# Kernel tuning notes

Measured on AMD Instinct MI355X. Metric: run time of the kernel, lower is better.

## Reference

```python
import jax, jax.numpy as jnp
import numpy as np

B_, S_, D_ = 2, 1024, 1024
EXPAND = 2
D_INNER = EXPAND * D_            # 2048
HEADDIM = 64
NHEADS = D_INNER // HEADDIM      # 32
D_STATE = 64
NGROUPS = 1
D_CONV = 4
CONV_DIM = D_INNER + 2 * NGROUPS * D_STATE      # 2176
D_IN_PROJ = 2 * D_INNER + 2 * NGROUPS * D_STATE + NHEADS  # 4256
H_MLP = 8 * D_                   # GatedMLP fc_1 out (scale * d_model)


def setup_inputs() -> dict:
    key = jax.random.key(0)
    ks = jax.random.split(key, 12)
    n = lambda k, shp, s=0.02: jax.random.normal(k, shp, dtype=jnp.float32) * s
    return {
        "x": jax.random.normal(ks[0], (B_, S_, D_), dtype=jnp.float32),
        "in_proj_w": n(ks[1], (D_IN_PROJ, D_)),
        "conv_w": n(ks[2], (CONV_DIM, D_CONV), 0.2),
        "conv_b": jnp.zeros((CONV_DIM,), jnp.float32),
        "dt_bias": jax.random.normal(ks[3], (NHEADS,), dtype=jnp.float32) * 0.5 - 2.0,
        "A_log": jnp.log(1.0 + 15.0 * jax.random.uniform(ks[4], (NHEADS,), dtype=jnp.float32)),
        "D": jax.random.normal(ks[5], (NHEADS,), dtype=jnp.float32) * 0.1 + 1.0,
        "ssm_norm_w": jnp.ones((D_INNER,), jnp.float32),
        "out_proj_w": n(ks[6], (D_, D_INNER)),
        "rms_w": jnp.ones((D_,), jnp.float32),
        "fc1_w": n(ks[7], (H_MLP, D_)),
        "fc2_w": n(ks[8], (D_, H_MLP // 2)),
    }


def _rms(x, w, eps=1e-5):
    return x * jax.lax.rsqrt(jnp.mean(x * x, axis=-1, keepdims=True) + eps) * w


def _mamba(x, in_proj_w, conv_w, conv_b, dt_bias, A_log, D, ssm_norm_w, out_proj_w):
    b, s, _ = x.shape
    zxbcdt = x @ in_proj_w.T                         # [b,s,D_IN_PROJ]
    z = zxbcdt[..., :D_INNER]
    xBC = zxbcdt[..., D_INNER:D_INNER + CONV_DIM]
    dt_raw = zxbcdt[..., -NHEADS:]
    # causal depthwise conv1d + SiLU
    xc = jnp.pad(jnp.transpose(xBC, (0, 2, 1)), ((0, 0), (0, 0), (D_CONV - 1, 0)))
    xc = jax.lax.conv_general_dilated(xc, conv_w[:, None, :], (1,), 'VALID',
                                      feature_group_count=CONV_DIM,
                                      dimension_numbers=('NCH', 'OIH', 'NCH'))
    xBC = jax.nn.silu(jnp.transpose(xc, (0, 2, 1)) + conv_b)
    xs = xBC[..., :D_INNER].reshape(b, s, NHEADS, HEADDIM)
    Bm = xBC[..., D_INNER:D_INNER + D_STATE]         # [b,s,n] (ngroups=1)
    Cm = xBC[..., D_INNER + D_STATE:]
    dt = jax.nn.softplus(dt_raw + dt_bias)           # [b,s,h]
    dA = jnp.exp(dt * (-jnp.exp(A_log)))             # [b,s,h]
    dtx = dt[..., None] * xs                          # [b,s,h,p]

    def step(h, inp):
        dA_t, dtx_t, B_t, C_t = inp
        h = h * dA_t[:, :, None, None] + jnp.einsum('bhp,bn->bhpn', dtx_t, B_t)
        y = jnp.einsum('bhpn,bn->bhp', h, C_t)
        return h, y

    h0 = jnp.zeros((b, NHEADS, HEADDIM, D_STATE), x.dtype)
    _, y = jax.lax.scan(step, h0, (jnp.transpose(dA, (1, 0, 2)),
                                   jnp.transpose(dtx, (1, 0, 2, 3)),
                                   jnp.transpose(Bm, (1, 0, 2)),
                                   jnp.transpose(Cm, (1, 0, 2))))
    y = jnp.transpose(y, (1, 0, 2, 3)) + D[None, None, :, None] * xs
    y = y.reshape(b, s, D_INNER) * jax.nn.silu(z)    # gated
    y = _rms(y, ssm_norm_w)
    return y @ out_proj_w.T


def reference(x, in_proj_w, conv_w, conv_b, dt_bias, A_log, D, ssm_norm_w,
              out_proj_w, rms_w, fc1_w, fc2_w):
    # x = x + mamba(x)
    x = x + _mamba(x, in_proj_w, conv_w, conv_b, dt_bias, A_log, D, ssm_norm_w, out_proj_w)
    # x = x + GatedMLP(RMSNorm(x))
    xn = _rms(x, rms_w)
    h1 = xn @ fc1_w.T
    a, g = jnp.split(h1, 2, axis=-1)
    m = (a * jax.nn.silu(g)) @ fc2_w.T
    return x + m
```

## Files before the change

kernel.cpp:

```cpp
#include <hip/hip_runtime.h>
#include <math.h>

typedef unsigned short u16;
typedef __attribute__((ext_vector_type(8))) __bf16 bf16x8;
typedef __attribute__((ext_vector_type(4))) float f32x4;
typedef __attribute__((ext_vector_type(4))) u16 u16x4;
typedef __attribute__((ext_vector_type(8))) u16 u16x8;
typedef __attribute__((ext_vector_type(4))) float float4v;

constexpr int kS = 1024;
constexpr int kD = 1024;
constexpr int kDinner = 2048;
constexpr int kHeads = 32;
constexpr int kConvDim = 2176;
constexpr int kDproj = 4256;
constexpr int kDprojPad = 4352;
constexpr int kRows = 2048;
constexpr int kHmlp = 8192;
constexpr int kHhalf = 4096;
constexpr int kL = 64;
constexpr int kNC = 16;

__device__ __forceinline__ float bf2f(u16 u) {
    return __builtin_bit_cast(float, (unsigned int)u << 16);
}
__device__ __forceinline__ u16 f2bf(float f) {
    unsigned int u = __builtin_bit_cast(unsigned int, f);
    u += 0x7fffu + ((u >> 16) & 1u);
    return (u16)(u >> 16);
}
__device__ __forceinline__ float silu_(float x) { return x / (1.f + __expf(-x)); }

__device__ __forceinline__ void gld16(const u16* g, u16* l) {
    __builtin_amdgcn_global_load_lds(
        (const __attribute__((address_space(1))) void*)g,
        (__attribute__((address_space(3))) void*)l, 16, 0, 0);
}

constexpr int kB1 = kRows * kD / 4;
constexpr int kB2 = kB1 + kDprojPad * kD / 4;
constexpr int kB3 = kB2 + kD * kDinner / 4;
constexpr int kB4 = kB3 + kHmlp * kD / 4;
constexpr int kB5 = kB4 + kD * kHhalf / 4;
__global__ __launch_bounds__(256)
void cast_all_kernel(const float* __restrict__ x, const float* __restrict__ w1,
                     const float* __restrict__ w2, const float* __restrict__ w3,
                     const float* __restrict__ w4, u16* __restrict__ xbf,
                     u16* __restrict__ w1bf, u16* __restrict__ w2bf,
                     u16* __restrict__ w3bf, u16* __restrict__ w4bf) {
    int i = blockIdx.x * 256 + threadIdx.x;
    const float* src;
    u16* dst;
    int j;
    if (i < kB1) {
        j = i; src = x; dst = xbf;
    } else if (i < kB2) {
        j = i - kB1;
        int e = j * 4, row = e >> 10, col = e & 1023;
        u16x4 o = {0, 0, 0, 0};
        if (row < kDproj) {
            float4v v = *(const float4v*)(w1 + (size_t)row * kD + col);
            o.x = f2bf(v.x); o.y = f2bf(v.y); o.z = f2bf(v.z); o.w = f2bf(v.w);
        }
        ((u16x4*)w1bf)[j] = o;
        return;
    } else if (i < kB3) {
        j = i - kB2; src = w2; dst = w2bf;
    } else if (i < kB4) {
        j = i - kB3;
        int e = j * 4, row = e >> 10, col4 = (e & 1023) >> 2;
        int p = (row < kHhalf) ? row : row - kHhalf;
        int permrow = (p >> 4) * 32 + (p & 15) + ((row < kHhalf) ? 0 : 16);
        float4v v = ((const float4v*)w3)[j];
        u16x4 o;
        o.x = f2bf(v.x); o.y = f2bf(v.y); o.z = f2bf(v.z); o.w = f2bf(v.w);
        ((u16x4*)w3bf)[permrow * 256 + col4] = o;
        return;
    } else {
        j = i - kB4; src = w4; dst = w4bf;
    }
    float4v v = ((const float4v*)src)[j];
    u16x4 o;
    o.x = f2bf(v.x); o.y = f2bf(v.y); o.z = f2bf(v.z); o.w = f2bf(v.w);
    ((u16x4*)dst)[j] = o;
}

template <bool OUT_BF16, bool GATED = false>
__global__ __launch_bounds__(256)
void gemm_bt(const u16* __restrict__ A, const u16* __restrict__ W,
             void* __restrict__ Cout, const float* __restrict__ resid,
             int M, int N, int K) {
    __shared__ u16 As[2][128 * 32];
    __shared__ u16 Bs[2][128 * 32];
    const int tid = threadIdx.x;
    const int lane = tid & 63;
    const int w = __builtin_amdgcn_readfirstlane(tid >> 6);
    const int wm = w >> 1, wn = w & 1;
    const int bm = blockIdx.y * 128;
    const int bn = blockIdx.x * 128;
    const int z = blockIdx.z;
    const int Kchunk = K / gridDim.z;
    const int k0 = z * Kchunk;

    f32x4 acc[4][4];
#pragma unroll
    for (int i = 0; i < 4; i++)
#pragma unroll
        for (int j = 0; j < 4; j++) acc[i][j] = {0.f, 0.f, 0.f, 0.f};

    const int srow = lane >> 2;
    const int scol = (lane & 3) * 8;
    const u16* gA = A + (size_t)(bm + w * 32 + srow) * K + k0 + scol;
    const u16* gB = W + (size_t)(bn + w * 32 + srow) * K + k0 + scol;
    const size_t rstep = (size_t)16 * K;

    const int sbase0 = (w * 32) * 32;
    const int sbase1 = (w * 32 + 16) * 32;
    const int fra = (lane & 15) * 32 + (lane >> 4) * 8;

    gld16(gA, &As[0][sbase0]);
    gld16(gA + rstep, &As[0][sbase1]);
    gld16(gB, &Bs[0][sbase0]);
    gld16(gB + rstep, &Bs[0][sbase1]);

    const int nk = Kchunk >> 5;
    for (int i = 0; i < nk; i++) {
        const int cur = i & 1, nxt = cur ^ 1;
        __syncthreads();
        if (i + 1 < nk) {
            int kt2 = (i + 1) * 32;
            gld16(gA + kt2, &As[nxt][sbase0]);
            gld16(gA + kt2 + rstep, &As[nxt][sbase1]);
            gld16(gB + kt2, &Bs[nxt][sbase0]);
            gld16(gB + kt2 + rstep, &Bs[nxt][sbase1]);
        }
        bf16x8 av[4], bv[4];
#pragma unroll
        for (int mi = 0; mi < 4; mi++)
            av[mi] = *(const bf16x8*)&As[cur][(wm * 64 + mi * 16) * 32 + fra];
#pragma unroll
        for (int ni = 0; ni < 4; ni++)
            bv[ni] = *(const bf16x8*)&Bs[cur][(wn * 64 + ni * 16) * 32 + fra];
#pragma unroll
        for (int mi = 0; mi < 4; mi++)
#pragma unroll
            for (int ni = 0; ni < 4; ni++)
                acc[mi][ni] = __builtin_amdgcn_mfma_f32_16x16x32_bf16(av[mi], bv[ni], acc[mi][ni], 0, 0, 0);
    }

    const int rb = bm + wm * 64 + ((lane >> 4) << 2);
    const int cb = bn + wn * 64 + (lane & 15);
    if (GATED) {
        u16* Cb = (u16*)Cout;
        const int NG = N >> 1;
        const int gc0 = ((bn + wn * 64) >> 1) + (lane & 15);
#pragma unroll
        for (int mi = 0; mi < 4; mi++) {
#pragma unroll
            for (int p = 0; p < 2; p++) {
#pragma unroll
                for (int r = 0; r < 4; r++) {
                    float a = acc[mi][2 * p][r];
                    float g = acc[mi][2 * p + 1][r];
                    Cb[(size_t)(rb + mi * 16 + r) * NG + gc0 + p * 16] =
                        f2bf(a * silu_(g));
                }
            }
        }
        return;
    }
    float* Cf = (float*)Cout + (size_t)z * M * N;
    u16* Cb = (u16*)Cout;
#pragma unroll
    for (int mi = 0; mi < 4; mi++) {
#pragma unroll
        for (int ni = 0; ni < 4; ni++) {
#pragma unroll
            for (int r = 0; r < 4; r++) {
                size_t offo = (size_t)(rb + mi * 16 + r) * N + (cb + ni * 16);
                float v = acc[mi][ni][r];
                if (resid) v += resid[offo];
                if (OUT_BF16) Cb[offo] = f2bf(v);
                else Cf[offo] = v;
            }
        }
    }
}

#define VMCNT6 asm volatile("s_waitcnt vmcnt(6)" ::: "memory")
#define VMCNT0 asm volatile("s_waitcnt vmcnt(0)" ::: "memory")

__global__ __launch_bounds__(512, 2)
void gemm256_gated(const u16* __restrict__ A, const u16* __restrict__ W,
                   u16* __restrict__ Cout, int M, int N, int K) {
    __shared__ u16 lds[2][2][2][2][4096];
    const int tid = threadIdx.x;
    const int lane = tid & 63;
    const int w = __builtin_amdgcn_readfirstlane(tid >> 6);
    const int wm = w >> 2;
    const int wn = w & 3;
    const int wnh = wn >> 1, wnl = wn & 1;

    const int ntn = N >> 8;
    const int ntiles = (M >> 8) * ntn;
    const int qchunk = ntiles >> 3;
    const int lin = blockIdx.x;
    const int swz = (lin & 7) * qchunk + (lin >> 3);
    const int bm = (swz / ntn) << 8;
    const int bn = (swz % ntn) << 8;

    const int rst = tid >> 2, sst = tid & 3;
    const int vst = (((rst >> 1) & 1) << 1) | ((rst >> 2) & 1);
    const u16* gA0 = A + (size_t)(bm + rst) * K + ((sst ^ vst) << 3);
    const u16* gB0 = W + (size_t)(bn + rst) * K + ((sst ^ vst) << 3);
    const size_t hstep = (size_t)128 * K;
    const int wq512 = w * 512;

    const int r0a = lane & 15, slot = lane >> 4;
    const int v2a = (((r0a >> 1) & 1) << 1) | ((r0a >> 2) & 1);
    const int fro = r0a * 32 + ((slot ^ v2a) << 3);

    f32x4 acc[8][4];
#pragma unroll
    for (int i = 0; i < 8; i++)
#pragma unroll
        for (int j = 0; j < 4; j++) acc[i][j] = {0.f, 0.f, 0.f, 0.f};
    bf16x8 bv[4];
    const int nt = K >> 6;

#define STAGE(d, mat, kh, kt)                                               \
    { const u16* g_ = ((mat) ? gB0 : gA0) + (size_t)(kt) * 64 + (kh) * 32;  \
      gld16(g_, &lds[d][mat][0][kh][wq512]);                                \
      gld16(g_ + hstep, &lds[d][mat][1][kh][wq512]); }

#define LDA_FRAG(dst, d, kh, mfb)                                           \
    _Pragma("unroll") for (int i_ = 0; i_ < 4; i_++)                        \
        dst[i_] = *(const bf16x8*)&lds[d][0][wm][kh][((mfb) + i_) * 512 + fro];

#define LDB_FRAG(d, kh)                                                     \
    _Pragma("unroll") for (int i_ = 0; i_ < 4; i_++)                        \
        bv[i_] = *(const bf16x8*)&lds[d][1][wnh][kh][wnl * 2048 + i_ * 512 + fro];

#define PHASE_TAIL(g4)                                                      \
    __builtin_amdgcn_sched_barrier(0);                                      \
    __builtin_amdgcn_s_barrier();                                           \
    __builtin_amdgcn_sched_barrier(0);                                      \
    __builtin_amdgcn_s_setprio(1);                                          \
    _Pragma("unroll") for (int i_ = 0; i_ < 4; i_++)                        \
        _Pragma("unroll") for (int n_ = 0; n_ < 4; n_++)                    \
            acc[(g4) * 4 + i_][n_] = __builtin_amdgcn_mfma_f32_16x16x32_bf16( \
                av[i_], bv[n_], acc[(g4) * 4 + i_][n_], 0, 0, 0);           \
    __builtin_amdgcn_s_setprio(0);                                          \
    __builtin_amdgcn_sched_barrier(0);                                      \
    __builtin_amdgcn_s_barrier();                                           \
    __builtin_amdgcn_sched_barrier(0);

#define TILE(T, D)                                                          \
    {                                             \
      { bf16x8 av[4]; LDB_FRAG(D, 0); LDA_FRAG(av, D, 0, 0);                \
        if ((T) + 1 < nt) STAGE(D ^ 1, 0, 1, (T) + 1);                      \
        PHASE_TAIL(0) }                                                     \
                                                  \
      { bf16x8 av[4]; LDA_FRAG(av, D, 0, 4);                                \
        if ((T) + 2 < nt) STAGE(D, 1, 0, (T) + 2);                          \
        PHASE_TAIL(1) }                                                     \
                                                  \
      { bf16x8 av[4]; LDB_FRAG(D, 1); LDA_FRAG(av, D, 1, 0);                \
        if ((T) + 2 < nt) STAGE(D, 0, 0, (T) + 2);                          \
        PHASE_TAIL(0) }                                                     \
                                  \
      { bf16x8 av[4]; LDA_FRAG(av, D, 1, 4);                                \
        if ((T) + 2 < nt) STAGE(D, 1, 1, (T) + 2);                          \
        if ((T) + 2 < nt) { VMCNT6; } else if ((T) + 1 < nt) { VMCNT0; }    \
        PHASE_TAIL(1) }                                                     \
    }

    STAGE(0, 1, 0, 0);
    STAGE(0, 0, 0, 0);
    STAGE(0, 1, 1, 0);
    STAGE(0, 0, 1, 0);
    STAGE(1, 1, 0, 1);
    STAGE(1, 0, 0, 1);
    STAGE(1, 1, 1, 1);
    VMCNT6;
    __builtin_amdgcn_sched_barrier(0);
    __builtin_amdgcn_s_barrier();
    __builtin_amdgcn_sched_barrier(0);

    for (int tt = 0; tt < nt; tt += 2) {
        TILE(tt, 0)
        TILE(tt + 1, 1)
    }

#undef TILE
#undef PHASE_TAIL
#undef LDB_FRAG
#undef LDA_FRAG
#undef STAGE

    u16* Cb = Cout;
    const int NG = N >> 1;
    const int rb = bm + wm * 128 + ((lane >> 4) << 2);
    const int gc0 = ((bn + wn * 64) >> 1) + (lane & 15);
#pragma unroll
    for (int mf = 0; mf < 8; mf++) {
#pragma unroll
        for (int p = 0; p < 2; p++) {
#pragma unroll
            for (int r = 0; r < 4; r++) {
                float a = acc[mf][2 * p][r];
                float g = acc[mf][2 * p + 1][r];
                Cb[(size_t)(rb + mf * 16 + r) * NG + gc0 + p * 16] =
                    f2bf(a * silu_(g));
            }
        }
    }
}

__global__ __launch_bounds__(256)
void splitk_reduce_kernel(const float* __restrict__ Cp, const float* __restrict__ resid,
                          float* __restrict__ out, int mn4) {
    int i = blockIdx.x * 256 + threadIdx.x;
    if (i >= mn4) return;
    constexpr size_t MN = (size_t)kRows * kD;
    float4v s0 = ((const float4v*)Cp)[i];
    float4v s1 = ((const float4v*)(Cp + MN))[i];
    float4v s2 = ((const float4v*)(Cp + 2 * MN))[i];
    float4v s3 = ((const float4v*)(Cp + 3 * MN))[i];
    float4v r = ((const float4v*)resid)[i];
    float4v o;
    o.x = s0.x + s1.x + s2.x + s3.x + r.x;
    o.y = s0.y + s1.y + s2.y + s3.y + r.y;
    o.z = s0.z + s1.z + s2.z + s3.z + r.z;
    o.w = s0.w + s1.w + s2.w + s3.w + r.w;
    ((float4v*)out)[i] = o;
}

__global__ __launch_bounds__(256)
void reduce_rms_kernel(const float* __restrict__ Cp, const float* __restrict__ resid,
                       float* __restrict__ x2, const float* __restrict__ rmsw,
                       u16* __restrict__ xnbf) {
    const int row = blockIdx.x;
    const int tid = threadIdx.x;
    constexpr size_t MN = (size_t)kRows * kD;
    size_t i = (size_t)row * (kD / 4) + tid;
    float4v s0 = ((const float4v*)Cp)[i];
    float4v s1 = ((const float4v*)(Cp + MN))[i];
    float4v s2 = ((const float4v*)(Cp + 2 * MN))[i];
    float4v s3 = ((const float4v*)(Cp + 3 * MN))[i];
    float4v r = ((const float4v*)resid)[i];
    float4v v;
    v.x = s0.x + s1.x + s2.x + s3.x + r.x;
    v.y = s0.y + s1.y + s2.y + s3.y + r.y;
    v.z = s0.z + s1.z + s2.z + s3.z + r.z;
    v.w = s0.w + s1.w + s2.w + s3.w + r.w;
    ((float4v*)x2)[i] = v;
    float ss = v.x * v.x + v.y * v.y + v.z * v.z + v.w * v.w;
#pragma unroll
    for (int off = 32; off > 0; off >>= 1) ss += __shfl_down(ss, off);
    __shared__ float red[4];
    int wv = tid >> 6, lane = tid & 63;
    if (lane == 0) red[wv] = ss;
    __syncthreads();
    ss = red[0] + red[1] + red[2] + red[3];
    float rstd = rsqrtf(ss * (1.f / kD) + 1e-5f);
    float4v wv4 = ((const float4v*)rmsw)[tid];
    u16x4 o;
    o.x = f2bf(v.x * rstd * wv4.x);
    o.y = f2bf(v.y * rstd * wv4.y);
    o.z = f2bf(v.z * rstd * wv4.z);
    o.w = f2bf(v.w * rstd * wv4.w);
    ((u16x4*)xnbf)[i] = o;
}

__global__ __launch_bounds__(256)
void convdt_kernel(const u16* __restrict__ zxbf, const float* __restrict__ convw,
                   const float* __restrict__ convb, u16* __restrict__ xsbf,
                   float* __restrict__ BCf, const float* __restrict__ dt_bias,
                   const float* __restrict__ A_log, float* __restrict__ dtf,
                   float* __restrict__ dAf) {
    int c = blockIdx.x * 256 + threadIdx.x;
    int row = blockIdx.y;
    if (c >= kConvDim + kHeads) return;
    if (c < kConvDim) {
        int s = row & (kS - 1);
        float acc = convb[c];
#pragma unroll
        for (int j = 0; j < 4; j++) {
            int sj = s - 3 + j;
            if (sj >= 0)
                acc += bf2f(zxbf[(size_t)(row - 3 + j) * kDprojPad + kDinner + c]) * convw[c * 4 + j];
        }
        float v = silu_(acc);
        if (c < kDinner) xsbf[(size_t)row * kDinner + c] = f2bf(v);
        else BCf[(size_t)row * 128 + (c - kDinner)] = v;
    } else {
        int h = c - kConvDim;
        float raw = bf2f(zxbf[(size_t)row * kDprojPad + (kDinner + kConvDim) + h]) + dt_bias[h];
        float dt = (raw > 20.f) ? raw : log1pf(__expf(raw));
        float dA = __expf(-dt * __expf(A_log[h]));
        dtf[(size_t)row * kHeads + h] = dt;
        dAf[(size_t)row * kHeads + h] = dA;
    }
}

__global__ __launch_bounds__(256)
void scan_chunk_kernel(const u16* __restrict__ xsbf, const float* __restrict__ BCf,
                       const float* __restrict__ dtf, const float* __restrict__ dAf,
                       const float* __restrict__ Dv, u16* __restrict__ ysbf,
                       float* __restrict__ Pf, float* __restrict__ Scf) {
    const int c = blockIdx.x, h = blockIdx.y, b = blockIdx.z;
    const int tid = threadIdx.x;
    const int lane = tid & 63;
    const int nq = tid >> 6;
    const int p = nq * 16 + (lane & 15);
    const int ng = lane >> 4;

    __shared__ float BC_lds[kL * 136];
    __shared__ u16 xs_lds[kL * 64];
    __shared__ float dA_lds[kL];
    __shared__ float dt_lds[kL];
    __shared__ u16 ybuf[kL * 64];

    const int row0 = b * kS + c * kL;

#pragma unroll
    for (int i = 0; i < 8; i++) {
        int e4 = i * 256 + tid;
        int t = e4 >> 5;
        int col = (e4 & 31) * 4;
        float4v v = *(const float4v*)(BCf + (size_t)(row0 + t) * 128 + col);
        int dst = t * 136 + (col < 64 ? col : col + 4);
        *(float4v*)&BC_lds[dst] = v;
    }
#pragma unroll
    for (int i = 0; i < 2; i++) {
        int e8 = i * 256 + tid;
        int t = e8 >> 3, col8 = (e8 & 7) * 8;
        *(u16x8*)&xs_lds[t * 64 + col8] =
            *(const u16x8*)(xsbf + (size_t)(row0 + t) * kDinner + h * 64 + col8);
    }
    if (tid < kL) {
        dt_lds[tid] = dtf[(size_t)(row0 + tid) * kHeads + h];
        dA_lds[tid] = dAf[(size_t)(row0 + tid) * kHeads + h];
    }
    __syncthreads();

    float hst[16];
#pragma unroll
    for (int j = 0; j < 16; j++) hst[j] = 0.f;
    float P = 1.f;
    const float Dh = Dv[h];

    for (int t = 0; t < kL; t++) {
        float dAv = dA_lds[t];
        float dtv = dt_lds[t];
        float xsv = bf2f(xs_lds[t * 64 + p]);
        float dtx = dtv * xsv;
        P *= dAv;
        const float* Bt = &BC_lds[t * 136 + ng * 16];
        const float* Ct = Bt + 68;
        float yp = 0.f;
#pragma unroll
        for (int j = 0; j < 16; j++) {
            float Bn = Bt[j];
            float Cn = Ct[j];
            hst[j] = hst[j] * dAv + dtx * Bn;
            yp += hst[j] * Cn;
        }
        yp += __shfl_xor(yp, 16);
        yp += __shfl_xor(yp, 32);
        if (ng == 0) ybuf[t * 64 + p] = f2bf(yp + Dh * xsv);
        if (tid == 0) Pf[(size_t)(row0 + t) * kHeads + h] = P;
    }
    __syncthreads();

#pragma unroll
    for (int i = 0; i < 2; i++) {
        int e8 = i * 256 + tid;
        int t = e8 >> 3, col8 = (e8 & 7) * 8;
        *(u16x8*)(ysbf + (size_t)(row0 + t) * kDinner + h * 64 + col8) =
            *(u16x8*)&ybuf[t * 64 + col8];
    }
    const int bhc = (b * 32 + h) * kNC + c;
    float* Sdst = Scf + (size_t)bhc * 4096 + p * 64 + ng * 16;
#pragma unroll
    for (int j = 0; j < 16; j += 4) {
        f32x4 v = {hst[j], hst[j + 1], hst[j + 2], hst[j + 3]};
        *(f32x4*)(Sdst + j) = v;
    }
}

__global__ __launch_bounds__(256)
void chunk_state_kernel(const float* __restrict__ Scf, const float* __restrict__ Pf,
                        float* __restrict__ Hinf) {
    const int bh = blockIdx.x;
    const int b = bh >> 5, h = bh & 31;
    const int tid = threadIdx.x;
    float hreg[16];
#pragma unroll
    for (int k = 0; k < 16; k++) hreg[k] = 0.f;
    for (int c = 0; c < kNC - 1; c++) {
        float Q = Pf[(size_t)(b * kS + c * kL + kL - 1) * kHeads + h];
        size_t sbase = (size_t)(bh * kNC + c) * 4096;
        size_t dbase = (size_t)(bh * kNC + c + 1) * 4096;
#pragma unroll
        for (int k = 0; k < 16; k++) {
            float s = Scf[sbase + k * 256 + tid];
            hreg[k] = Q * hreg[k] + s;
            Hinf[dbase + k * 256 + tid] = hreg[k];
        }
    }
}

__global__ __launch_bounds__(256)
void chunk_corr_kernel(const float* __restrict__ Hinf, const float* __restrict__ BCf,
                       const float* __restrict__ Pf, u16* __restrict__ ysbf) {
    const int c = blockIdx.x + 1;
    const int h = blockIdx.y, b = blockIdx.z;
    const int tid = threadIdx.x;
    const int lane = tid & 63, wq = tid >> 6;
    __shared__ float Hin_lds[64 * 65];
    __shared__ float C_lds[kL * 64];
    const int bh = b * 32 + h;
    const size_t hbase = (size_t)(bh * kNC + c) * 4096;
#pragma unroll
    for (int k = 0; k < 16; k++) {
        int e = k * 256 + tid;
        Hin_lds[(e >> 6) * 65 + (e & 63)] = Hinf[hbase + e];
    }
    const int row0 = b * kS + c * kL;
#pragma unroll
    for (int k = 0; k < 4; k++) {
        int e4 = k * 256 + tid;
        int t = e4 >> 4, n4 = (e4 & 15) * 4;
        *(float4v*)&C_lds[t * 64 + n4] =
            *(const float4v*)(BCf + (size_t)(row0 + t) * 128 + 64 + n4);
    }
    __syncthreads();

    float hr[64];
#pragma unroll
    for (int n = 0; n < 64; n++) hr[n] = Hin_lds[lane * 65 + n];

    for (int tt = 0; tt < 16; tt++) {
        int t = wq * 16 + tt;
        float corr = 0.f;
#pragma unroll
        for (int n4 = 0; n4 < 16; n4++) {
            float4v cv = *(const float4v*)&C_lds[t * 64 + n4 * 4];
            corr += cv.x * hr[n4 * 4] + cv.y * hr[n4 * 4 + 1] +
                    cv.z * hr[n4 * 4 + 2] + cv.w * hr[n4 * 4 + 3];
        }
        float Pt = Pf[(size_t)(row0 + t) * kHeads + h];
        size_t yoff = (size_t)(row0 + t) * kDinner + h * 64 + lane;
        ysbf[yoff] = f2bf(bf2f(ysbf[yoff]) + Pt * corr);
    }
}

__global__ __launch_bounds__(256)
void gatenorm_kernel(const u16* __restrict__ ysbf, const u16* __restrict__ zxbf,
                     const float* __restrict__ normw, u16* __restrict__ ybf) {
    const int row = blockIdx.x;
    const int tid = threadIdx.x;
    float v[8];
    float ss = 0.f;
#pragma unroll
    for (int i = 0; i < 8; i++) {
        int idx = i * 256 + tid;
        float y = bf2f(ysbf[(size_t)row * kDinner + idx]);
        float z = bf2f(zxbf[(size_t)row * kDprojPad + idx]);
        v[i] = y * silu_(z);
        ss += v[i] * v[i];
    }
#pragma unroll
    for (int off = 32; off > 0; off >>= 1) ss += __shfl_down(ss, off);
    __shared__ float red[4];
    int wv = tid >> 6, lane = tid & 63;
    if (lane == 0) red[wv] = ss;
    __syncthreads();
    ss = red[0] + red[1] + red[2] + red[3];
    float rstd = rsqrtf(ss * (1.f / kDinner) + 1e-5f);
#pragma unroll
    for (int i = 0; i < 8; i++) {
        int idx = i * 256 + tid;
        ybf[(size_t)row * kDinner + idx] = f2bf(v[i] * rstd * normw[idx]);
    }
}

extern "C" void kernel_launch(void* const* d_in, const int* in_sizes, int n_in,
                              void* d_out, int out_size, void* d_ws, size_t ws_size,
                              hipStream_t stream) {
    const float* x         = (const float*)d_in[0];
    const float* in_proj_w = (const float*)d_in[1];
    const float* conv_w    = (const float*)d_in[2];
    const float* conv_b    = (const float*)d_in[3];
    const float* dt_bias   = (const float*)d_in[4];
    const float* A_log     = (const float*)d_in[5];
    const float* Dvec      = (const float*)d_in[6];
    const float* ssm_norm_w= (const float*)d_in[7];
    const float* out_proj_w= (const float*)d_in[8];
    const float* rms_w     = (const float*)d_in[9];
    const float* fc1_w     = (const float*)d_in[10];
    const float* fc2_w     = (const float*)d_in[11];
    float* out = (float*)d_out;

    char* ws = (char*)d_ws;
    size_t off = 0;
    auto alloc = [&](size_t bytes) -> void* {
        void* p = ws + off;
        off += (bytes + 255) & ~(size_t)255;
        return p;
    };
    u16*   xbf  = (u16*)alloc((size_t)kRows * kD * 2);
    u16*   w1bf = (u16*)alloc((size_t)kDprojPad * kD * 2);
    u16*   w2bf = (u16*)alloc((size_t)kD * kDinner * 2);
    u16*   w3bf = (u16*)alloc((size_t)kHmlp * kD * 2);
    u16*   w4bf = (u16*)alloc((size_t)kD * kHhalf * 2);
    u16*   zxbf = (u16*)alloc((size_t)kRows * kDprojPad * 2);
    u16*   xsbf = (u16*)alloc((size_t)kRows * kDinner * 2);
    float* BCf  = (float*)alloc((size_t)kRows * 128 * 4);
    float* dtf  = (float*)alloc((size_t)kRows * kHeads * 4);
    float* dAf  = (float*)alloc((size_t)kRows * kHeads * 4);
    float* Pf   = (float*)alloc((size_t)kRows * kHeads * 4);
    u16*   ysbf = (u16*)alloc((size_t)kRows * kDinner * 2);
    u16*   ybf  = (u16*)alloc((size_t)kRows * kDinner * 2);
    float* x2   = (float*)alloc((size_t)kRows * kD * 4);
    u16*   xnbf = (u16*)alloc((size_t)kRows * kD * 2);
    u16*   h1bf = (u16*)alloc((size_t)kRows * kHmlp * 2);
    u16*   gbf  = (u16*)alloc((size_t)kRows * kHhalf * 2);
    float* Scf  = (float*)gbf;
    float* Hinf = (float*)h1bf;
    float* Cp   = (float*)h1bf;
    (void)ws_size; (void)in_sizes; (void)n_in; (void)out_size;

    cast_all_kernel<<<kB5 / 256, 256, 0, stream>>>(
        x, in_proj_w, out_proj_w, fc1_w, fc2_w, xbf, w1bf, w2bf, w3bf, w4bf);

    gemm_bt<true><<<dim3(kDprojPad / 128, kRows / 128, 1), 256, 0, stream>>>(
        xbf, w1bf, zxbf, nullptr, kRows, kDprojPad, kD);

    convdt_kernel<<<dim3((kConvDim + kHeads + 255) / 256, kRows), 256, 0, stream>>>(
        zxbf, conv_w, conv_b, xsbf, BCf, dt_bias, A_log, dtf, dAf);

    scan_chunk_kernel<<<dim3(kNC, kHeads, 2), 256, 0, stream>>>(
        xsbf, BCf, dtf, dAf, Dvec, ysbf, Pf, Scf);
    chunk_state_kernel<<<64, 256, 0, stream>>>(Scf, Pf, Hinf);
    chunk_corr_kernel<<<dim3(kNC - 1, kHeads, 2), 256, 0, stream>>>(Hinf, BCf, Pf, ysbf);

    gatenorm_kernel<<<kRows, 256, 0, stream>>>(ysbf, zxbf, ssm_norm_w, ybf);

    gemm_bt<false><<<dim3(kD / 128, kRows / 128, 4), 256, 0, stream>>>(
        ybf, w2bf, Cp, nullptr, kRows, kD, kDinner);
    reduce_rms_kernel<<<kRows, 256, 0, stream>>>(Cp, x, x2, rms_w, xnbf);

    gemm256_gated<<<dim3((kRows >> 8) * (kHmlp >> 8)), 512, 0, stream>>>(
        xnbf, w3bf, gbf, kRows, kHmlp, kD);

    gemm_bt<false><<<dim3(kD / 128, kRows / 128, 4), 256, 0, stream>>>(
        gbf, w4bf, Cp, nullptr, kRows, kD, kHhalf);
    splitk_reduce_kernel<<<(kRows * kD / 4 + 255) / 256, 256, 0, stream>>>(
        Cp, x2, out, kRows * kD / 4);
}
```

Baseline: 372.0 us.

## Relax gated GEMM pipeline waits, drop sched barriers, remap tiles per XCD

The gated fc1 GEMM's software pipeline is reworked. Global-load waits move after the MFMA block and are loosened (vmcnt 10 instead of 6), with an extra wait in the second phase. Explicit lgkmcnt waits replace the sched_barrier fences, so the compiler can interleave more freely. The block-to-tile mapping is also changed to a fixed 2D XCD-aware layout so each XCD works on a compact 4x8 tile region for L2 reuse. The intent is more overlap of loads with MFMAs and better cache locality. The risks are a hardcoded grid shape and possible data races if the vmcnt accounting is wrong.

```diff
diff --git a/kernel.cpp b/kernel.cpp
--- a/kernel.cpp
+++ b/kernel.cpp
@@ -187,8 +187,8 @@
     }
 }
 
-#define VMCNT6 asm volatile("s_waitcnt vmcnt(6)" ::: "memory")
-#define VMCNT0 asm volatile("s_waitcnt vmcnt(0)" ::: "memory")
+#define VMCNT10 asm volatile("s_waitcnt vmcnt(10)" ::: "memory")
+#define VMCNT0  asm volatile("s_waitcnt vmcnt(0)" ::: "memory")
 
 __global__ __launch_bounds__(512, 2)
 void gemm256_gated(const u16* __restrict__ A, const u16* __restrict__ W,
@@ -201,13 +201,10 @@
     const int wn = w & 3;
     const int wnh = wn >> 1, wnl = wn & 1;
 
-    const int ntn = N >> 8;
-    const int ntiles = (M >> 8) * ntn;
-    const int qchunk = ntiles >> 3;
     const int lin = blockIdx.x;
-    const int swz = (lin & 7) * qchunk + (lin >> 3);
-    const int bm = (swz / ntn) << 8;
-    const int bn = (swz % ntn) << 8;
+    const int xcd = lin & 7, j = lin >> 3;
+    const int bm = (((xcd >> 2) << 2) + (j & 3)) << 8;
+    const int bn = (((xcd & 3) << 3) + (j >> 2)) << 8;
 
     const int rst = tid >> 2, sst = tid & 3;
     const int vst = (((rst >> 1) & 1) << 1) | ((rst >> 2) & 1);
@@ -224,7 +221,7 @@
 #pragma unroll
     for (int i = 0; i < 8; i++)
 #pragma unroll
-        for (int j = 0; j < 4; j++) acc[i][j] = {0.f, 0.f, 0.f, 0.f};
+        for (int j_ = 0; j_ < 4; j_++) acc[i][j_] = {0.f, 0.f, 0.f, 0.f};
     bf16x8 bv[4];
     const int nt = K >> 6;
 
@@ -241,38 +238,36 @@
     _Pragma("unroll") for (int i_ = 0; i_ < 4; i_++)                        \
         bv[i_] = *(const bf16x8*)&lds[d][1][wnh][kh][wnl * 2048 + i_ * 512 + fro];
 
-#define PHASE_TAIL(g4)                                                      \
-    __builtin_amdgcn_sched_barrier(0);                                      \
+#define PHASE_TAIL(g4, ...)                                                 \
     __builtin_amdgcn_s_barrier();                                           \
-    __builtin_amdgcn_sched_barrier(0);                                      \
+    asm volatile("s_waitcnt lgkmcnt(0)" ::: "memory");                      \
     __builtin_amdgcn_s_setprio(1);                                          \
     _Pragma("unroll") for (int i_ = 0; i_ < 4; i_++)                        \
         _Pragma("unroll") for (int n_ = 0; n_ < 4; n_++)                    \
             acc[(g4) * 4 + i_][n_] = __builtin_amdgcn_mfma_f32_16x16x32_bf16( \
                 av[i_], bv[n_], acc[(g4) * 4 + i_][n_], 0, 0, 0);           \
     __builtin_amdgcn_s_setprio(0);                                          \
-    __builtin_amdgcn_sched_barrier(0);                                      \
-    __builtin_amdgcn_s_barrier();                                           \
-    __builtin_amdgcn_sched_barrier(0);
+    __VA_ARGS__;                                                            \
+    __builtin_amdgcn_s_barrier();
 
 #define TILE(T, D)                                                          \
     {                                             \
       { bf16x8 av[4]; LDB_FRAG(D, 0); LDA_FRAG(av, D, 0, 0);                \
         if ((T) + 1 < nt) STAGE(D ^ 1, 0, 1, (T) + 1);                      \
-        PHASE_TAIL(0) }                                                     \
-                                                  \
+        PHASE_TAIL(0, ((void)0)) }                                          \
+                                             \
       { bf16x8 av[4]; LDA_FRAG(av, D, 0, 4);                                \
         if ((T) + 2 < nt) STAGE(D, 1, 0, (T) + 2);                          \
-        PHASE_TAIL(1) }                                                     \
+        PHASE_TAIL(1, if ((T) + 2 < nt) { VMCNT10; } else { VMCNT0; }) }    \
                                                   \
       { bf16x8 av[4]; LDB_FRAG(D, 1); LDA_FRAG(av, D, 1, 0);                \
         if ((T) + 2 < nt) STAGE(D, 0, 0, (T) + 2);                          \
-        PHASE_TAIL(0) }                                                     \
-                                  \
+        PHASE_TAIL(0, ((void)0)) }                                          \
+                                             \
       { bf16x8 av[4]; LDA_FRAG(av, D, 1, 4);                                \
         if ((T) + 2 < nt) STAGE(D, 1, 1, (T) + 2);                          \
-        if ((T) + 2 < nt) { VMCNT6; } else if ((T) + 1 < nt) { VMCNT0; }    \
-        PHASE_TAIL(1) }                                                     \
+        PHASE_TAIL(1, if ((T) + 2 < nt) { VMCNT10; }                        \
+                      else if ((T) + 1 < nt) { VMCNT0; }) }                 \
     }
 
     STAGE(0, 1, 0, 0);
@@ -282,10 +277,8 @@
     STAGE(1, 1, 0, 1);
     STAGE(1, 0, 0, 1);
     STAGE(1, 1, 1, 1);
-    VMCNT6;
-    __builtin_amdgcn_sched_barrier(0);
+    VMCNT10;
     __builtin_amdgcn_s_barrier();
-    __builtin_amdgcn_sched_barrier(0);
 
     for (int tt = 0; tt < nt; tt += 2) {
         TILE(tt, 0)
```

After: 366.2 us. Within noise of the previous version (-1.6%).
